# Optimization experiments

Hardware: AMD Instinct MI355X
Metric: run time of the kernel (lower is better)

## Reference

```python
import jax, jax.numpy as jnp
import numpy as np
import math

# config constants (match init_kwargs)
H = 1024; NH = 16; NKV = 4; HD = 64; E = 16; I = 512
NG = 4; TKG = 2; TK = 4; ROUTED_SCALE = 2.5; EPS = 1e-6; THETA = 10000.0
B = 2; S = 1024


def setup_inputs() -> dict:
    key = jax.random.key(0)
    ks = jax.random.split(key, 16)
    sd = 0.02
    inp = {
        "hidden_states": jax.random.normal(ks[0], (B, S, H), jnp.float32),
        "position_ids": jnp.arange(B * S, dtype=jnp.int64).reshape(B, S) % 4096,
        "ln1_w": jnp.ones((H,), jnp.float32),
        "ln2_w": jnp.ones((H,), jnp.float32),
        "q_w": jax.random.normal(ks[1], (NH * HD, H), jnp.float32) * sd,
        "k_w": jax.random.normal(ks[2], (NKV * HD, H), jnp.float32) * sd,
        "v_w": jax.random.normal(ks[3], (NKV * HD, H), jnp.float32) * sd,
        "o_w": jax.random.normal(ks[4], (H, NH * HD), jnp.float32) * sd,
        "gate_w": jax.random.normal(ks[5], (E, H), jnp.float32) * sd,
        "e_bias": jax.random.normal(ks[6], (E,), jnp.float32) * 0.1,
        "W_gu": jax.random.normal(ks[7], (E, 2 * I, H), jnp.float32) * sd,
        "W_d": jax.random.normal(ks[8], (E, H, I), jnp.float32) * sd,
        "sg_w": jax.random.normal(ks[9], (2 * I, H), jnp.float32) * sd,
        "su_w": jax.random.normal(ks[10], (2 * I, H), jnp.float32) * sd,
        "sd_w": jax.random.normal(ks[11], (H, 2 * I), jnp.float32) * sd,
    }
    return inp


def _rmsnorm(x, w, eps=EPS):
    v = jnp.mean(x.astype(jnp.float32) ** 2, axis=-1, keepdims=True)
    return w * (x * jax.lax.rsqrt(v + eps)).astype(w.dtype)


def _rotate_half(x):
    x1, x2 = x[..., : HD // 2], x[..., HD // 2 :]
    return jnp.concatenate([-x2, x1], axis=-1)


def _attention(hs, position_ids, q_w, k_w, v_w, o_w):
    b, s, _ = hs.shape
    q = (hs @ q_w.T).reshape(b, s, NH, HD).transpose(0, 2, 1, 3)   # [B,NH,S,HD]
    k = (hs @ k_w.T).reshape(b, s, NKV, HD).transpose(0, 2, 1, 3)
    v = (hs @ v_w.T).reshape(b, s, NKV, HD).transpose(0, 2, 1, 3)
    # RoPE
    inv_freq = 1.0 / (THETA ** (jnp.arange(0, HD, 2, dtype=jnp.float32) / HD))
    freqs = position_ids.astype(jnp.float32)[..., None] * inv_freq  # [B,S,HD/2]
    emb = jnp.concatenate([freqs, freqs], axis=-1)                  # [B,S,HD]
    cos = jnp.cos(emb)[:, None]                                     # [B,1,S,HD]
    sin = jnp.sin(emb)[:, None]
    q = q * cos + _rotate_half(q) * sin
    k = k * cos + _rotate_half(k) * sin
    # GQA: repeat kv heads
    groups = NH // NKV
    k = jnp.repeat(k, groups, axis=1)
    v = jnp.repeat(v, groups, axis=1)
    scale = 1.0 / math.sqrt(HD)
    scores = jnp.einsum("bhsd,bhtd->bhst", q, k) * scale
    causal = jnp.triu(jnp.full((s, s), -jnp.inf, jnp.float32), k=1)
    scores = scores + causal[None, None]
    attn = jax.nn.softmax(scores.astype(jnp.float32), axis=-1).astype(q.dtype)
    out = jnp.einsum("bhst,bhtd->bhsd", attn, v)
    out = out.transpose(0, 2, 1, 3).reshape(b, s, NH * HD)
    return out @ o_w.T


def _moe(x, gate_w, e_bias, W_gu, W_d, sg_w, su_w, sd_w):
    b, s, h = x.shape
    xf = x.reshape(-1, h)                                     # [T,H]
    T = xf.shape[0]
    logits = xf.astype(jnp.float32) @ gate_w.astype(jnp.float32).T  # [T,E]
    scores = jax.nn.sigmoid(logits)
    sfc = scores + e_bias[None]
    # group-restricted top-k
    gsize = E // NG
    group_scores = sfc.reshape(T, NG, gsize).max(axis=-1)     # [T,NG]
    _, gidx = jax.lax.top_k(group_scores, TKG)                # [T,TKG]
    gmask = jnp.zeros((T, NG), bool).at[jnp.arange(T)[:, None], gidx].set(True)
    smask = jnp.repeat(gmask, gsize, axis=1)                  # [T,E]
    masked = jnp.where(smask, sfc, 0.0)
    _, topk_idx = jax.lax.top_k(masked, TK)                   # [T,TK]
    topk_w = jnp.take_along_axis(scores, topk_idx, axis=1)    # [T,TK]
    topk_w = topk_w / (topk_w.sum(axis=-1, keepdims=True) + 1e-20)
    topk_w = (topk_w * ROUTED_SCALE).astype(xf.dtype)
    # combine weights [T,E] (scatter-add over selected experts)
    combine = jnp.zeros((T, E), xf.dtype).at[
        jnp.arange(T)[:, None], topk_idx].add(topk_w)
    # dense expert compute (static shapes), weighted combine fused in einsum
    gu = jnp.einsum("th,eih->tei", xf, W_gu)                  # [T,E,2I]
    hidden = jax.nn.silu(gu[..., :I]) * gu[..., I:]           # [T,E,I]
    routed = jnp.einsum("tei,ehi,te->th", hidden, W_d, combine)
    # shared experts
    shared = ((jax.nn.silu(xf @ sg_w.T) * (xf @ su_w.T)) @ sd_w.T)
    return (routed + shared).reshape(b, s, h)


def reference(hidden_states, position_ids, ln1_w, ln2_w, q_w, k_w, v_w, o_w,
              gate_w, e_bias, W_gu, W_d, sg_w, su_w, sd_w):
    res = hidden_states
    hs = _rmsnorm(hidden_states, ln1_w)
    hs = res + _attention(hs, position_ids, q_w, k_w, v_w, o_w)
    res = hs
    hs = _rmsnorm(hs, ln2_w)
    hs = res + _moe(hs, gate_w, e_bias, W_gu, W_d, sg_w, su_w, sd_w)
    return hs
```

## Files before the change

kernel.cpp:

```cpp
#include <hip/hip_runtime.h>
#include <hip/hip_bf16.h>
#include <stdint.h>

typedef float f32x4 __attribute__((ext_vector_type(4)));
typedef short s16x8 __attribute__((ext_vector_type(8)));
typedef short s16x4 __attribute__((ext_vector_type(4)));

__device__ __forceinline__ short f2bf(float x) {
    union { float f; uint32_t u; } v; v.f = x;
    uint32_t r = v.u + 0x7fffu + ((v.u >> 16) & 1u);
    return (short)(r >> 16);
}
__device__ __forceinline__ float bf2f(short b) {
    union { uint32_t u; float f; } v; v.u = ((uint32_t)(uint16_t)b) << 16;
    return v.f;
}
__device__ __forceinline__ void gld16(const void* g, void* l) {
    __builtin_amdgcn_global_load_lds((const __attribute__((address_space(1))) uint32_t*)g,
                                     (__attribute__((address_space(3))) uint32_t*)l, 16, 0, 0);
}

__global__ __launch_bounds__(256) void cvt_small_kernel(const float* __restrict__ q, const float* __restrict__ k,
                                                        const float* __restrict__ v, const float* __restrict__ sg,
                                                        const float* __restrict__ su, short* __restrict__ wqkv,
                                                        short* __restrict__ wsgsu) {
    size_t i = (size_t)blockIdx.x * 256 + threadIdx.x;
    const float* src; short* dst;
    if (i < 131072) { src = q + i * 8; dst = wqkv + i * 8; }
    else if (i < 163840) { src = k + (i - 131072) * 8; dst = wqkv + 1048576 + (i - 131072) * 8; }
    else if (i < 196608) { src = v + (i - 163840) * 8; dst = wqkv + 1310720 + (i - 163840) * 8; }
    else if (i < 327680) { src = sg + (i - 196608) * 8; dst = wsgsu + (i - 196608) * 8; }
    else { src = su + (i - 327680) * 8; dst = wsgsu + 1048576 + (i - 327680) * 8; }
    f32x4 a = ((const f32x4*)src)[0];
    f32x4 b = ((const f32x4*)src)[1];
    s16x8 o8;
    o8[0] = f2bf(a[0]); o8[1] = f2bf(a[1]); o8[2] = f2bf(a[2]); o8[3] = f2bf(a[3]);
    o8[4] = f2bf(b[0]); o8[5] = f2bf(b[1]); o8[6] = f2bf(b[2]); o8[7] = f2bf(b[3]);
    *(s16x8*)dst = o8;
}

__global__ __launch_bounds__(256) void rmsnorm_kernel(const float* __restrict__ x, const float* __restrict__ w,
                                                      short* __restrict__ out) {
    int t = blockIdx.x;
    f32x4 v = ((const f32x4*)(x + (size_t)t * 1024))[threadIdx.x];
    float ssq = v[0]*v[0] + v[1]*v[1] + v[2]*v[2] + v[3]*v[3];
#pragma unroll
    for (int o = 1; o < 64; o <<= 1) ssq += __shfl_xor(ssq, o);
    __shared__ float red[4];
    if ((threadIdx.x & 63) == 0) red[threadIdx.x >> 6] = ssq;
    __syncthreads();
    float tot = red[0] + red[1] + red[2] + red[3];
    float rs = rsqrtf(tot * (1.0f / 1024.0f) + 1e-6f);
    f32x4 wv = ((const f32x4*)w)[threadIdx.x];
    s16x4 o4;
#pragma unroll
    for (int j = 0; j < 4; ++j) o4[j] = f2bf(v[j] * rs * wv[j]);
    ((s16x4*)(out + (size_t)t * 1024))[threadIdx.x] = o4;
}

__global__ __launch_bounds__(256) void addnorm_kernel(const float* __restrict__ a, const short* __restrict__ b,
                                                      const float* __restrict__ w, float* __restrict__ res,
                                                      short* __restrict__ xf, float* __restrict__ xf32) {
    int t = blockIdx.x;
    f32x4 va = ((const f32x4*)(a + (size_t)t * 1024))[threadIdx.x];
    f32x4 vb = {0.f, 0.f, 0.f, 0.f};
#pragma unroll
    for (int z = 0; z < 4; ++z) {
        s16x4 dz = *(const s16x4*)(b + (size_t)z * 2048 * 1024 + (size_t)t * 1024 + threadIdx.x * 4);
#pragma unroll
        for (int j = 0; j < 4; ++j) vb[j] += bf2f(dz[j]);
    }
    f32x4 s = va + vb;
    ((f32x4*)(res + (size_t)t * 1024))[threadIdx.x] = s;
    float ssq = s[0]*s[0] + s[1]*s[1] + s[2]*s[2] + s[3]*s[3];
#pragma unroll
    for (int o = 1; o < 64; o <<= 1) ssq += __shfl_xor(ssq, o);
    __shared__ float red[4];
    if ((threadIdx.x & 63) == 0) red[threadIdx.x >> 6] = ssq;
    __syncthreads();
    float tot = red[0] + red[1] + red[2] + red[3];
    float rs = rsqrtf(tot * (1.0f / 1024.0f) + 1e-6f);
    f32x4 wv = ((const f32x4*)w)[threadIdx.x];
    f32x4 xo;
    s16x4 o4;
#pragma unroll
    for (int j = 0; j < 4; ++j) { xo[j] = s[j] * rs * wv[j]; o4[j] = f2bf(xo[j]); }
    ((f32x4*)(xf32 + (size_t)t * 1024))[threadIdx.x] = xo;
    ((s16x4*)(xf + (size_t)t * 1024))[threadIdx.x] = o4;
}

__global__ __launch_bounds__(256, 4) void gemm2_kernel(const short* __restrict__ A, const short* __restrict__ Bg,
                                                       void* __restrict__ Cv, int M, int N, int Ktot, int Ksub,
                                                       long long cstride,
                                                       const int* __restrict__ counts, const int* __restrict__ lists,
                                                       const int* __restrict__ plan, int a_shift, int store_bf16) {
    __shared__ short As[2][128 * 32];
    __shared__ short Bs[2][128 * 32];
    int e, bm, bn, k0, Mloc;
    size_t coff = (size_t)blockIdx.z * cstride;
    const int* rl = nullptr;
    if (plan) {
        int wi = blockIdx.y;
        if (wi >= plan[0]) return;
        int it = plan[1 + wi];
        e = it & 31; bm = (it >> 5) * 128;
        bn = blockIdx.x * 128;
        Mloc = counts[e]; rl = lists + e * 2048;
    } else {
        e = 0; bm = blockIdx.x * 128; bn = blockIdx.y * 128;
        Mloc = M;
    }
    k0 = blockIdx.z * Ksub;
    if (bm >= Mloc) return;
    const short* Bt = Bg + (size_t)e * N * Ktot;
    int tid = threadIdx.x, w = tid >> 6, l = tid & 63;
    int lr = l & 15, lg = l >> 4;
    int rsub = l >> 2, u = l & 3;
    int fs = (rsub & 3) ^ ((rsub >> 2) & 3);
    int colsel = (u ^ fs) * 8;
    int ra = w * 32 + rsub;
    int ga0 = bm + ra;       if (ga0 > Mloc - 1) ga0 = Mloc - 1;
    int ga1 = bm + ra + 16;  if (ga1 > Mloc - 1) ga1 = Mloc - 1;
    int ar0 = rl ? (rl[ga0] >> a_shift) : ga0;
    int ar1 = rl ? (rl[ga1] >> a_shift) : ga1;
    const short* Ap0 = A + (size_t)ar0 * Ktot + k0 + colsel;
    const short* Ap1 = A + (size_t)ar1 * Ktot + k0 + colsel;
    const short* Bp0 = Bt + (size_t)(bn + ra) * Ktot + k0 + colsel;
    const short* Bp1 = Bt + (size_t)(bn + ra + 16) * Ktot + k0 + colsel;
    int lb0 = w * 1024, lb1 = w * 1024 + 512;

    int wm = (w >> 1) * 64, wn = (w & 1) * 64;
    int su = lg ^ (lr & 3) ^ ((lr >> 2) & 3);
    int aoff[4], boff[4];
#pragma unroll
    for (int mf = 0; mf < 4; ++mf) aoff[mf] = (wm + mf * 16 + lr) * 32 + su * 8;
#pragma unroll
    for (int nf = 0; nf < 4; ++nf) boff[nf] = (wn + nf * 16 + lr) * 32 + su * 8;

    f32x4 zero4 = {0.f, 0.f, 0.f, 0.f};
    f32x4 acc[4][4];
#pragma unroll
    for (int mf = 0; mf < 4; ++mf)
#pragma unroll
        for (int nf = 0; nf < 4; ++nf) acc[mf][nf] = zero4;

#define STAGE(buf, kt) do { \
        gld16(Ap0 + (kt) * 32, &As[buf][lb0]); \
        gld16(Ap1 + (kt) * 32, &As[buf][lb1]); \
        gld16(Bp0 + (kt) * 32, &Bs[buf][lb0]); \
        gld16(Bp1 + (kt) * 32, &Bs[buf][lb1]); \
    } while (0)

    int nk = Ksub >> 5;
    STAGE(0, 0);
    asm volatile("s_waitcnt vmcnt(0)");
    __syncthreads();
    for (int kt = 0; kt < nk; ++kt) {
        int cur = kt & 1;
        if (kt + 1 < nk) STAGE(cur ^ 1, kt + 1);
        s16x8 af[4], bfr[4];
#pragma unroll
        for (int mf = 0; mf < 4; ++mf) af[mf] = *(const s16x8*)&As[cur][aoff[mf]];
#pragma unroll
        for (int nf = 0; nf < 4; ++nf) bfr[nf] = *(const s16x8*)&Bs[cur][boff[nf]];
#pragma unroll
        for (int mf = 0; mf < 4; ++mf)
#pragma unroll
            for (int nf = 0; nf < 4; ++nf)
                acc[mf][nf] = __builtin_amdgcn_mfma_f32_16x16x32_bf16(af[mf], bfr[nf], acc[mf][nf], 0, 0, 0);
        __syncthreads();
    }
#undef STAGE
    float* Cf = (float*)Cv;
    short* Cs = (short*)Cv;
#pragma unroll
    for (int mf = 0; mf < 4; ++mf) {
        int rbase = bm + wm + mf * 16 + lg * 4;
#pragma unroll
        for (int r = 0; r < 4; ++r) {
            int grow = rbase + r;
            if (grow < Mloc) {
                int crow = rl ? rl[grow] : grow;
                size_t cb = coff + (size_t)crow * N + bn + wn + lr;
                if (store_bf16) {
#pragma unroll
                    for (int nf = 0; nf < 4; ++nf) Cs[cb + nf * 16] = f2bf(acc[mf][nf][r]);
                } else {
#pragma unroll
                    for (int nf = 0; nf < 4; ++nf) Cf[cb + nf * 16] = acc[mf][nf][r];
                }
            }
        }
    }
}

__global__ __launch_bounds__(256, 3) void gemm3_kernel(const short* __restrict__ A, const float* __restrict__ Bg,
                                                       void* __restrict__ Cv, int M, int N, int Ktot, int Ksub,
                                                       long long cstride,
                                                       const int* __restrict__ counts, const int* __restrict__ lists,
                                                       const int* __restrict__ plan, int a_shift, int store_bf16) {
    __shared__ short As[2][128 * 32];
    __shared__ short Bs[2][128 * 32];
    int e, bm, bn, k0, Mloc;
    size_t coff = (size_t)blockIdx.z * cstride;
    const int* rl = nullptr;
    if (plan) {
        int wi = blockIdx.y;
        if (wi >= plan[0]) return;
        int it = plan[1 + wi];
        e = it & 31; bm = (it >> 5) * 128;
        bn = blockIdx.x * 128;
        Mloc = counts[e]; rl = lists + e * 2048;
    } else {
        e = 0; bm = blockIdx.x * 128; bn = blockIdx.y * 128;
        Mloc = M;
    }
    k0 = blockIdx.z * Ksub;
    if (bm >= Mloc) return;
    const float* Bt = Bg + (size_t)e * N * Ktot;
    int tid = threadIdx.x, w = tid >> 6, l = tid & 63;
    int lr = l & 15, lg = l >> 4;
    int rsub = l >> 2, u = l & 3;
    int fs = (rsub & 3) ^ ((rsub >> 2) & 3);
    int colsel = (u ^ fs) * 8;
    int ra = w * 32 + rsub;
    int ga0 = bm + ra;       if (ga0 > Mloc - 1) ga0 = Mloc - 1;
    int ga1 = bm + ra + 16;  if (ga1 > Mloc - 1) ga1 = Mloc - 1;
    int ar0 = rl ? (rl[ga0] >> a_shift) : ga0;
    int ar1 = rl ? (rl[ga1] >> a_shift) : ga1;
    const short* Ap0 = A + (size_t)ar0 * Ktot + k0 + colsel;
    const short* Ap1 = A + (size_t)ar1 * Ktot + k0 + colsel;
    const float* Bp0 = Bt + (size_t)(bn + ra) * Ktot + k0 + u * 8;
    const float* Bp1 = Bt + (size_t)(bn + ra + 16) * Ktot + k0 + u * 8;
    int lb0 = w * 1024, lb1 = w * 1024 + 512;
    int sb0 = w * 1024 + rsub * 32 + colsel, sb1 = sb0 + 512;

    int wm = (w >> 1) * 64, wn = (w & 1) * 64;
    int su = lg ^ (lr & 3) ^ ((lr >> 2) & 3);
    int aoff[4], boff[4];
#pragma unroll
    for (int mf = 0; mf < 4; ++mf) aoff[mf] = (wm + mf * 16 + lr) * 32 + su * 8;
#pragma unroll
    for (int nf = 0; nf < 4; ++nf) boff[nf] = (wn + nf * 16 + lr) * 32 + su * 8;

    f32x4 zero4 = {0.f, 0.f, 0.f, 0.f};
    f32x4 acc[4][4];
#pragma unroll
    for (int mf = 0; mf < 4; ++mf)
#pragma unroll
        for (int nf = 0; nf < 4; ++nf) acc[mf][nf] = zero4;

    f32x4 b00, b01, b10, b11;
#define BLOAD(kt) do { \
        const float* p0 = Bp0 + (kt) * 32; const float* p1 = Bp1 + (kt) * 32; \
        b00 = *(const f32x4*)p0; b01 = *(const f32x4*)(p0 + 4); \
        b10 = *(const f32x4*)p1; b11 = *(const f32x4*)(p1 + 4); \
    } while (0)
#define BWRITE(buf) do { \
        s16x8 t0, t1; \
        t0[0] = f2bf(b00[0]); t0[1] = f2bf(b00[1]); t0[2] = f2bf(b00[2]); t0[3] = f2bf(b00[3]); \
        t0[4] = f2bf(b01[0]); t0[5] = f2bf(b01[1]); t0[6] = f2bf(b01[2]); t0[7] = f2bf(b01[3]); \
        t1[0] = f2bf(b10[0]); t1[1] = f2bf(b10[1]); t1[2] = f2bf(b10[2]); t1[3] = f2bf(b10[3]); \
        t1[4] = f2bf(b11[0]); t1[5] = f2bf(b11[1]); t1[6] = f2bf(b11[2]); t1[7] = f2bf(b11[3]); \
        *(s16x8*)&Bs[buf][sb0] = t0; *(s16x8*)&Bs[buf][sb1] = t1; \
    } while (0)
#define ASTAGE(buf, kt) do { \
        gld16(Ap0 + (kt) * 32, &As[buf][lb0]); \
        gld16(Ap1 + (kt) * 32, &As[buf][lb1]); \
    } while (0)

    int nk = Ksub >> 5;
    BLOAD(0); ASTAGE(0, 0); BWRITE(0);
    asm volatile("s_waitcnt vmcnt(0)");
    __syncthreads();
    for (int kt = 0; kt < nk; ++kt) {
        int cur = kt & 1;
        if (kt + 1 < nk) { BLOAD(kt + 1); ASTAGE(cur ^ 1, kt + 1); }
        s16x8 af[4], bfr[4];
#pragma unroll
        for (int mf = 0; mf < 4; ++mf) af[mf] = *(const s16x8*)&As[cur][aoff[mf]];
#pragma unroll
        for (int nf = 0; nf < 4; ++nf) bfr[nf] = *(const s16x8*)&Bs[cur][boff[nf]];
#pragma unroll
        for (int mf = 0; mf < 4; ++mf)
#pragma unroll
            for (int nf = 0; nf < 4; ++nf)
                acc[mf][nf] = __builtin_amdgcn_mfma_f32_16x16x32_bf16(af[mf], bfr[nf], acc[mf][nf], 0, 0, 0);
        if (kt + 1 < nk) BWRITE(cur ^ 1);
        __syncthreads();
    }
#undef BLOAD
#undef BWRITE
#undef ASTAGE
    float* Cf = (float*)Cv;
    short* Cs = (short*)Cv;
#pragma unroll
    for (int mf = 0; mf < 4; ++mf) {
        int rbase = bm + wm + mf * 16 + lg * 4;
#pragma unroll
        for (int r = 0; r < 4; ++r) {
            int grow = rbase + r;
            if (grow < Mloc) {
                int crow = rl ? rl[grow] : grow;
                size_t cb = coff + (size_t)crow * N + bn + wn + lr;
                if (store_bf16) {
#pragma unroll
                    for (int nf = 0; nf < 4; ++nf) Cs[cb + nf * 16] = f2bf(acc[mf][nf][r]);
                } else {
#pragma unroll
                    for (int nf = 0; nf < 4; ++nf) Cf[cb + nf * 16] = acc[mf][nf][r];
                }
            }
        }
    }
}

__global__ __launch_bounds__(64) void rope_kernel(const short* __restrict__ qkv, short* __restrict__ Qr,
                                                  short* __restrict__ Kr, short* __restrict__ Vt) {
    int t = blockIdx.x;
    int b = t >> 10, s = t & 1023;
    int l = threadIdx.x;
    __shared__ float cs[32], sn[32], row[1536];
    float acc[24];
#pragma unroll
    for (int c = 0; c < 24; ++c) acc[c] = 0.f;
#pragma unroll
    for (int z = 0; z < 4; ++z) {
        const short* src = qkv + (size_t)z * 2048 * 1536 + (size_t)t * 1536 + l * 24;
#pragma unroll
        for (int c8 = 0; c8 < 3; ++c8) {
            s16x8 v8 = *(const s16x8*)(src + c8 * 8);
#pragma unroll
            for (int j = 0; j < 8; ++j) acc[c8 * 8 + j] += bf2f(v8[j]);
        }
    }
#pragma unroll
    for (int c = 0; c < 24; ++c) row[l * 24 + c] = acc[c];
    if (l < 32) {
        float fr = (float)t * exp2f(-(float)l * 0.41524101186f);
        cs[l] = cosf(fr); sn[l] = sinf(fr);
    }
    __syncthreads();
    int d = l;
    float c = cs[d & 31], sv = sn[d & 31];
#pragma unroll
    for (int h = 0; h < 16; ++h) {
        float x = row[h * 64 + d];
        float rot = (d < 32) ? -row[h * 64 + d + 32] : row[h * 64 + d - 32];
        Qr[((size_t)(b * 16 + h) * 1024 + s) * 64 + d] = f2bf((x * c + rot * sv) * 0.125f);
    }
#pragma unroll
    for (int h = 0; h < 4; ++h) {
        float x = row[1024 + h * 64 + d];
        float rot = (d < 32) ? -row[1024 + h * 64 + d + 32] : row[1024 + h * 64 + d - 32];
        Kr[((size_t)(b * 4 + h) * 1024 + s) * 64 + d] = f2bf(x * c + rot * sv);
        Vt[((size_t)(b * 4 + h) * 64 + d) * 1024 + s] = f2bf(row[1280 + h * 64 + d]);
    }
}

struct KV { s16x8 k[4]; s16x8 v[4]; };
__device__ __forceinline__ void kv_load(KV& r, const short* Kb, const short* Vb, int k0, int lr, int lg) {
    const short* K0 = Kb + (size_t)(k0 + lr) * 64 + lg * 8;
    const short* K1 = Kb + (size_t)(k0 + 16 + lr) * 64 + lg * 8;
    r.k[0] = *(const s16x8*)K0;
    r.k[1] = *(const s16x8*)(K0 + 32);
    r.k[2] = *(const s16x8*)K1;
    r.k[3] = *(const s16x8*)(K1 + 32);
#pragma unroll
    for (int dt = 0; dt < 4; ++dt)
        r.v[dt] = *(const s16x8*)(Vb + (size_t)(dt * 16 + lr) * 1024 + k0 + lg * 8);
}
__device__ __forceinline__ void chain_step(const KV& kv, s16x8 qf0, s16x8 qf1, f32x4* o,
                                           float& m, float& lsum, short* Pl,
                                           int lr, int lg, int k0, int qmask) {
    f32x4 z = {0.f, 0.f, 0.f, 0.f};
    f32x4 sc0 = z, sc1 = z;
    sc0 = __builtin_amdgcn_mfma_f32_16x16x32_bf16(kv.k[0], qf0, sc0, 0, 0, 0);
    sc0 = __builtin_amdgcn_mfma_f32_16x16x32_bf16(kv.k[1], qf1, sc0, 0, 0, 0);
    sc1 = __builtin_amdgcn_mfma_f32_16x16x32_bf16(kv.k[2], qf0, sc1, 0, 0, 0);
    sc1 = __builtin_amdgcn_mfma_f32_16x16x32_bf16(kv.k[3], qf1, sc1, 0, 0, 0);
#pragma unroll
    for (int r = 0; r < 4; ++r) {
        if (k0 + lg * 4 + r > qmask) sc0[r] = -1e30f;
        if (k0 + 16 + lg * 4 + r > qmask) sc1[r] = -1e30f;
    }
    float tm = fmaxf(fmaxf(fmaxf(sc0[0], sc0[1]), fmaxf(sc0[2], sc0[3])),
                     fmaxf(fmaxf(sc1[0], sc1[1]), fmaxf(sc1[2], sc1[3])));
    tm = fmaxf(tm, __shfl_xor(tm, 16));
    tm = fmaxf(tm, __shfl_xor(tm, 32));
    float newm = fmaxf(m, tm);
    float fac = __expf(m - newm);
    float p[8];
#pragma unroll
    for (int r = 0; r < 4; ++r) { p[r] = __expf(sc0[r] - newm); p[4 + r] = __expf(sc1[r] - newm); }
    float ts = ((p[0] + p[1]) + (p[2] + p[3])) + ((p[4] + p[5]) + (p[6] + p[7]));
    ts += __shfl_xor(ts, 16);
    ts += __shfl_xor(ts, 32);
    lsum = lsum * fac + ts;
    m = newm;
    s16x4 w0, w1;
#pragma unroll
    for (int r = 0; r < 4; ++r) { w0[r] = f2bf(p[r]); w1[r] = f2bf(p[4 + r]); }
    *(s16x4*)&Pl[lr * 40 + lg * 4] = w0;
    *(s16x4*)&Pl[lr * 40 + 16 + lg * 4] = w1;
    s16x8 pf = *(const s16x8*)&Pl[lr * 40 + lg * 8];
#pragma unroll
    for (int dt = 0; dt < 4; ++dt) {
        o[dt] *= fac;
        o[dt] = __builtin_amdgcn_mfma_f32_16x16x32_bf16(kv.v[dt], pf, o[dt], 0, 0, 0);
    }
}

__global__ __launch_bounds__(64) void attn_kernel(const short* __restrict__ Qr, const short* __restrict__ Kr,
                                                  const short* __restrict__ Vt, short* __restrict__ attn_out) {
    int p = blockIdx.x;
    int hb = blockIdx.y;
    int b = hb >> 4, h = hb & 15, kv = h >> 2;
    int l = threadIdx.x;
    int lr = l & 15, lg = l >> 4;
    int q0A = p * 16, q0B = (63 - p) * 16;
    __shared__ short PlA[16 * 40], PlB[16 * 40];
    const short* Qh = Qr + (size_t)(b * 16 + h) * 1024 * 64;
    s16x8 qA0 = *(const s16x8*)(Qh + (size_t)(q0A + lr) * 64 + lg * 8);
    s16x8 qA1 = *(const s16x8*)(Qh + (size_t)(q0A + lr) * 64 + 32 + lg * 8);
    s16x8 qB0 = *(const s16x8*)(Qh + (size_t)(q0B + lr) * 64 + lg * 8);
    s16x8 qB1 = *(const s16x8*)(Qh + (size_t)(q0B + lr) * 64 + 32 + lg * 8);
    const short* Kbase = Kr + (size_t)(b * 4 + kv) * 1024 * 64;
    const short* Vbase = Vt + (size_t)(b * 4 + kv) * 64 * 1024;

    f32x4 zero4 = {0.f, 0.f, 0.f, 0.f};
    f32x4 oA[4], oB[4];
#pragma unroll
    for (int dt = 0; dt < 4; ++dt) { oA[dt] = zero4; oB[dt] = zero4; }
    float mA = -1e30f, lsA = 0.f, mB = -1e30f, lsB = 0.f;
    int ntA = (q0A + 47) >> 5, ntB = (q0B + 47) >> 5;
    int qmA = q0A + lr, qmB = q0B + lr;
    const int BIG = 1 << 29;

    KV b0, b1;
    kv_load(b0, Kbase, Vbase, 0, lr, lg);
    for (int kt = 0; kt < ntB; kt += 2) {
        if (kt + 1 < ntB) kv_load(b1, Kbase, Vbase, (kt + 1) * 32, lr, lg);
        if (kt < ntA) chain_step(b0, qA0, qA1, oA, mA, lsA, PlA, lr, lg, kt * 32,
                                 (kt == ntA - 1) ? qmA : BIG);
        chain_step(b0, qB0, qB1, oB, mB, lsB, PlB, lr, lg, kt * 32,
                   (kt == ntB - 1) ? qmB : BIG);
        if (kt + 1 >= ntB) break;
        if (kt + 2 < ntB) kv_load(b0, Kbase, Vbase, (kt + 2) * 32, lr, lg);
        if (kt + 1 < ntA) chain_step(b1, qA0, qA1, oA, mA, lsA, PlA, lr, lg, (kt + 1) * 32,
                                     (kt + 1 == ntA - 1) ? qmA : BIG);
        chain_step(b1, qB0, qB1, oB, mB, lsB, PlB, lr, lg, (kt + 1) * 32,
                   (kt + 1 == ntB - 1) ? qmB : BIG);
    }
    float invA = 1.f / lsA, invB = 1.f / lsB;
    short* oa = attn_out + ((size_t)(b * 1024 + q0A + lr)) * 1024 + h * 64;
    short* ob = attn_out + ((size_t)(b * 1024 + q0B + lr)) * 1024 + h * 64;
#pragma unroll
    for (int dt = 0; dt < 4; ++dt)
#pragma unroll
        for (int r = 0; r < 4; ++r) {
            oa[dt * 16 + lg * 4 + r] = f2bf(oA[dt][r] * invA);
            ob[dt * 16 + lg * 4 + r] = f2bf(oB[dt][r] * invB);
        }
}

__global__ __launch_bounds__(256) void router_topk_kernel(const float* __restrict__ x32, const float* __restrict__ gw,
                                                          const float* __restrict__ eb, float* __restrict__ tw,
                                                          int* __restrict__ tidx) {
    int t = blockIdx.x * 4 + (threadIdx.x >> 6);
    int l = threadIdx.x & 63;
    const float* x = x32 + (size_t)t * 1024;
    f32x4 xv[4];
#pragma unroll
    for (int j = 0; j < 4; ++j) xv[j] = *(const f32x4*)(x + j * 256 + l * 4);
    float acc[16];
#pragma unroll
    for (int e = 0; e < 16; ++e) {
        float a = 0.f;
#pragma unroll
        for (int j = 0; j < 4; ++j) {
            f32x4 g = *(const f32x4*)(gw + (size_t)e * 1024 + j * 256 + l * 4);
            a += xv[j][0]*g[0] + xv[j][1]*g[1] + xv[j][2]*g[2] + xv[j][3]*g[3];
        }
        acc[e] = a;
    }
#pragma unroll
    for (int e = 0; e < 16; ++e) {
#pragma unroll
        for (int o = 1; o < 64; o <<= 1) acc[e] += __shfl_xor(acc[e], o);
    }
    if (l == 0) {
        float score[16], sfc[16];
#pragma unroll
        for (int e = 0; e < 16; ++e) {
            score[e] = 1.f / (1.f + __expf(-acc[e]));
            sfc[e] = score[e] + eb[e];
        }
        float gs[4];
#pragma unroll
        for (int g = 0; g < 4; ++g)
            gs[g] = fmaxf(fmaxf(sfc[4 * g], sfc[4 * g + 1]), fmaxf(sfc[4 * g + 2], sfc[4 * g + 3]));
        int g1 = 0;
        for (int g = 1; g < 4; ++g) if (gs[g] > gs[g1]) g1 = g;
        int g2 = -1;
        for (int g = 0; g < 4; ++g) {
            if (g == g1) continue;
            if (g2 < 0 || gs[g] > gs[g2]) g2 = g;
        }
        float masked[16];
#pragma unroll
        for (int e = 0; e < 16; ++e) {
            int g = e >> 2;
            masked[e] = (g == g1 || g == g2) ? sfc[e] : 0.0f;
        }
        float tot = 1e-20f;
        int idx[4]; float wv[4];
        for (int k = 0; k < 4; ++k) {
            int bi = 0;
            float bv = -1e30f;
            for (int e2 = 0; e2 < 16; ++e2)
                if (masked[e2] > bv) { bv = masked[e2]; bi = e2; }
            idx[k] = bi;
            wv[k] = score[bi];
            masked[bi] = -1e30f;
            tot += wv[k];
        }
        for (int k = 0; k < 4; ++k) {
            tw[t * 4 + k] = wv[k] / tot * 2.5f;
            tidx[t * 4 + k] = idx[k];
        }
    }
}

__global__ __launch_bounds__(64) void router_lists_kernel(const int* __restrict__ tidx, int* __restrict__ counts,
                                                          int* __restrict__ lists) {
    int e = blockIdx.x;
    int l = threadIdx.x;
    int base = 0;
    for (int it = 0; it < 128; ++it) {
        int p = it * 64 + l;
        bool match = (tidx[p] == e);
        unsigned long long mask = __ballot(match);
        int pos = __popcll(mask & ((1ull << l) - 1ull));
        if (match) lists[e * 2048 + base + pos] = p;
        base += __popcll(mask);
    }
    if (l == 0) counts[e] = base;
}

__global__ void plan_kernel(const int* __restrict__ counts, int* __restrict__ plan) {
    if (threadIdx.x == 0) {
        int n = 0;
        for (int e = 0; e < 16; ++e) {
            int nb = (counts[e] + 127) >> 7;
            for (int m2 = 0; m2 < nb; ++m2) plan[1 + n++] = e | (m2 << 5);
        }
        plan[0] = n;
    }
}

__global__ __launch_bounds__(128) void silu_routed_kernel(const short* __restrict__ gu, short* __restrict__ hid) {
    int pr = blockIdx.x;
    int j = threadIdx.x * 4;
    float g[4] = {0.f, 0.f, 0.f, 0.f}, u2[4] = {0.f, 0.f, 0.f, 0.f};
#pragma unroll
    for (int z = 0; z < 2; ++z) {
        const short* base = gu + (size_t)z * 8192 * 1024 + (size_t)pr * 1024;
        s16x4 gz = *(const s16x4*)(base + j);
        s16x4 uz = *(const s16x4*)(base + 512 + j);
#pragma unroll
        for (int k = 0; k < 4; ++k) { g[k] += bf2f(gz[k]); u2[k] += bf2f(uz[k]); }
    }
    s16x4 o;
#pragma unroll
    for (int k = 0; k < 4; ++k) o[k] = f2bf(g[k] / (1.f + __expf(-g[k])) * u2[k]);
    *(s16x4*)(hid + (size_t)pr * 512 + j) = o;
}

__global__ __launch_bounds__(256) void silu_shared_kernel(const short* __restrict__ gu, short* __restrict__ h) {
    int t = blockIdx.x;
    int j = threadIdx.x * 4;
    float g[4] = {0.f, 0.f, 0.f, 0.f}, u2[4] = {0.f, 0.f, 0.f, 0.f};
#pragma unroll
    for (int z = 0; z < 2; ++z) {
        const short* base = gu + (size_t)z * 2048 * 2048 + (size_t)t * 2048;
        s16x4 gz = *(const s16x4*)(base + j);
        s16x4 uz = *(const s16x4*)(base + 1024 + j);
#pragma unroll
        for (int k = 0; k < 4; ++k) { g[k] += bf2f(gz[k]); u2[k] += bf2f(uz[k]); }
    }
    s16x4 o;
#pragma unroll
    for (int k = 0; k < 4; ++k) o[k] = f2bf(g[k] / (1.f + __expf(-g[k])) * u2[k]);
    *(s16x4*)(h + (size_t)t * 1024 + j) = o;
}

__global__ __launch_bounds__(256) void combine_kernel(const float* __restrict__ res2, const short* __restrict__ sdp,
                                                      const short* __restrict__ slots, const float* __restrict__ tw,
                                                      float* __restrict__ out) {
    int t = blockIdx.x;
    int i = threadIdx.x;
    f32x4 acc = ((const f32x4*)(res2 + (size_t)t * 1024))[i];
#pragma unroll
    for (int z = 0; z < 4; ++z) {
        s16x4 d = *(const s16x4*)(sdp + (size_t)z * 2048 * 1024 + (size_t)t * 1024 + i * 4);
#pragma unroll
        for (int j = 0; j < 4; ++j) acc[j] += bf2f(d[j]);
    }
#pragma unroll
    for (int s = 0; s < 4; ++s) {
        float w = tw[t * 4 + s];
        s16x4 d = ((const s16x4*)(slots + (size_t)(t * 4 + s) * 1024))[i];
#pragma unroll
        for (int j = 0; j < 4; ++j) acc[j] += bf2f(d[j]) * w;
    }
    ((f32x4*)(out + (size_t)t * 1024))[i] = acc;
}

extern "C" void kernel_launch(void* const* d_in, const int* in_sizes, int n_in,
                              void* d_out, int out_size, void* d_ws, size_t ws_size,
                              hipStream_t stream) {
    const float* hidden = (const float*)d_in[0];
    const float* ln1 = (const float*)d_in[2];
    const float* ln2 = (const float*)d_in[3];
    const float* qw = (const float*)d_in[4];
    const float* kw = (const float*)d_in[5];
    const float* vw = (const float*)d_in[6];
    const float* ow = (const float*)d_in[7];
    const float* gatew = (const float*)d_in[8];
    const float* ebias = (const float*)d_in[9];
    const float* wgu = (const float*)d_in[10];
    const float* wd = (const float*)d_in[11];
    const float* sgw = (const float*)d_in[12];
    const float* suw = (const float*)d_in[13];
    const float* sdw = (const float*)d_in[14];
    float* out = (float*)d_out;

    char* base = (char*)d_ws;
    size_t off = 0;
    auto alloc = [&](size_t bytes) -> char* {
        char* r = base + off;
        off += (bytes + 255) & ~(size_t)255;
        return r;
    };
    const size_t MB = 1u << 20;

    short* wqkv_b = (short*)alloc((size_t)1536 * 1024 * 2);
    short* wsgsu_b= (short*)alloc((size_t)2048 * 1024 * 2);
    float* res2 = (float*)alloc((size_t)2048 * 1024 * 4);
    short* xf   = (short*)alloc((size_t)2048 * 1024 * 2);
    float* topkw = (float*)alloc(2048 * 4 * 4);
    int* tidx   = (int*)alloc(8192 * 4);
    int* counts = (int*)alloc(64);
    int* lists  = (int*)alloc(16 * 2048 * 4);
    int* plan   = (int*)alloc(512);
    short* shhid = (short*)alloc((size_t)2048 * 1024 * 2);
    short* hid   = (short*)alloc((size_t)8192 * 512 * 2);

    char* ov = alloc(50 * MB);
    short* xn1       = (short*)(ov);
    short* qkv_part  = (short*)(ov + 4 * MB);
    short* Qr        = (short*)(ov);
    short* Kr        = (short*)(ov + 28 * MB);
    short* Vt        = (short*)(ov + 29 * MB);
    short* attn_out  = (short*)(ov + 30 * MB);
    short* attnproj_part = (short*)(ov + 34 * MB);
    float* xf32      = (float*)(ov);
    short* upbuf     = (short*)(ov);
    short* down_slot = (short*)(ov);
    short* sd_part   = (short*)(ov + 16 * MB);

    cvt_small_kernel<<<1792, 256, 0, stream>>>(qw, kw, vw, sgw, suw, wqkv_b, wsgsu_b);

    rmsnorm_kernel<<<2048, 256, 0, stream>>>(hidden, ln1, xn1);
    gemm2_kernel<<<dim3(16, 12, 4), 256, 0, stream>>>(xn1, wqkv_b, qkv_part, 2048, 1536, 1024, 256,
                                                      2048LL * 1536, nullptr, nullptr, nullptr, 0, 1);
    rope_kernel<<<2048, 64, 0, stream>>>(qkv_part, Qr, Kr, Vt);
    attn_kernel<<<dim3(32, 32, 1), 64, 0, stream>>>(Qr, Kr, Vt, attn_out);
    gemm3_kernel<<<dim3(16, 8, 4), 256, 0, stream>>>(attn_out, ow, attnproj_part, 2048, 1024, 1024, 256,
                                                     2048LL * 1024, nullptr, nullptr, nullptr, 0, 1);
    addnorm_kernel<<<2048, 256, 0, stream>>>(hidden, attnproj_part, ln2, res2, xf, xf32);

    router_topk_kernel<<<512, 256, 0, stream>>>(xf32, gatew, ebias, topkw, tidx);
    router_lists_kernel<<<16, 64, 0, stream>>>(tidx, counts, lists);
    plan_kernel<<<1, 64, 0, stream>>>(counts, plan);

    gemm2_kernel<<<dim3(16, 16, 2), 256, 0, stream>>>(xf, wsgsu_b, upbuf, 2048, 2048, 1024, 512,
                                                      2048LL * 2048, nullptr, nullptr, nullptr, 0, 1);
    silu_shared_kernel<<<2048, 256, 0, stream>>>(upbuf, shhid);

    gemm3_kernel<<<dim3(8, 80, 2), 256, 0, stream>>>(xf, wgu, upbuf, 0, 1024, 1024, 512,
                                                     8192LL * 1024, counts, lists, plan, 2, 1);
    silu_routed_kernel<<<8192, 128, 0, stream>>>(upbuf, hid);

    gemm3_kernel<<<dim3(8, 80, 1), 256, 0, stream>>>(hid, wd, down_slot, 0, 1024, 512, 512,
                                                     0LL, counts, lists, plan, 0, 1);
    gemm3_kernel<<<dim3(16, 8, 4), 256, 0, stream>>>(shhid, sdw, sd_part, 2048, 1024, 1024, 256,
                                                     2048LL * 1024, nullptr, nullptr, nullptr, 0, 1);

    combine_kernel<<<2048, 256, 0, stream>>>(res2, sd_part, down_slot, topkw, out);

    (void)in_sizes; (void)n_in; (void)out_size; (void)ws_size;
}
```

Measured before the change: 278.3 us.

## Deepen gemm3 B-register prefetch to two stages with partial vmcnt waits

```diff
diff --git a/kernel.cpp b/kernel.cpp
--- a/kernel.cpp
+++ b/kernel.cpp
@@ -194,7 +194,14 @@
     }
 }
 
-__global__ __launch_bounds__(256, 3) void gemm3_kernel(const short* __restrict__ A, const float* __restrict__ Bg,
+#define WAITBAR4 do { __builtin_amdgcn_sched_barrier(0); \
+        asm volatile("s_waitcnt vmcnt(4) lgkmcnt(0)" ::: "memory"); \
+        __builtin_amdgcn_s_barrier(); __builtin_amdgcn_sched_barrier(0); } while (0)
+#define WAITBAR0 do { __builtin_amdgcn_sched_barrier(0); \
+        asm volatile("s_waitcnt vmcnt(0) lgkmcnt(0)" ::: "memory"); \
+        __builtin_amdgcn_s_barrier(); __builtin_amdgcn_sched_barrier(0); } while (0)
+
+__global__ __launch_bounds__(256, 4) void gemm3_kernel(const short* __restrict__ A, const float* __restrict__ Bg,
                                                        void* __restrict__ Cv, int M, int N, int Ktot, int Ksub,
                                                        long long cstride,
                                                        const int* __restrict__ counts, const int* __restrict__ lists,
@@ -250,48 +257,60 @@
 #pragma unroll
         for (int nf = 0; nf < 4; ++nf) acc[mf][nf] = zero4;
 
-    f32x4 b00, b01, b10, b11;
-#define BLOAD(kt) do { \
+    f32x4 bA00, bA01, bA10, bA11, bB00, bB01, bB10, bB11;
+#define BLOAD(S, kt) do { \
         const float* p0 = Bp0 + (kt) * 32; const float* p1 = Bp1 + (kt) * 32; \
-        b00 = *(const f32x4*)p0; b01 = *(const f32x4*)(p0 + 4); \
-        b10 = *(const f32x4*)p1; b11 = *(const f32x4*)(p1 + 4); \
+        S##00 = *(const f32x4*)p0; S##01 = *(const f32x4*)(p0 + 4); \
+        S##10 = *(const f32x4*)p1; S##11 = *(const f32x4*)(p1 + 4); \
     } while (0)
-#define BWRITE(buf) do { \
+#define BWRITE(S, buf) do { \
         s16x8 t0, t1; \
-        t0[0] = f2bf(b00[0]); t0[1] = f2bf(b00[1]); t0[2] = f2bf(b00[2]); t0[3] = f2bf(b00[3]); \
-        t0[4] = f2bf(b01[0]); t0[5] = f2bf(b01[1]); t0[6] = f2bf(b01[2]); t0[7] = f2bf(b01[3]); \
-        t1[0] = f2bf(b10[0]); t1[1] = f2bf(b10[1]); t1[2] = f2bf(b10[2]); t1[3] = f2bf(b10[3]); \
-        t1[4] = f2bf(b11[0]); t1[5] = f2bf(b11[1]); t1[6] = f2bf(b11[2]); t1[7] = f2bf(b11[3]); \
+        t0[0] = f2bf(S##00[0]); t0[1] = f2bf(S##00[1]); t0[2] = f2bf(S##00[2]); t0[3] = f2bf(S##00[3]); \
+        t0[4] = f2bf(S##01[0]); t0[5] = f2bf(S##01[1]); t0[6] = f2bf(S##01[2]); t0[7] = f2bf(S##01[3]); \
+        t1[0] = f2bf(S##10[0]); t1[1] = f2bf(S##10[1]); t1[2] = f2bf(S##10[2]); t1[3] = f2bf(S##10[3]); \
+        t1[4] = f2bf(S##11[0]); t1[5] = f2bf(S##11[1]); t1[6] = f2bf(S##11[2]); t1[7] = f2bf(S##11[3]); \
         *(s16x8*)&Bs[buf][sb0] = t0; *(s16x8*)&Bs[buf][sb1] = t1; \
     } while (0)
 #define ASTAGE(buf, kt) do { \
         gld16(Ap0 + (kt) * 32, &As[buf][lb0]); \
         gld16(Ap1 + (kt) * 32, &As[buf][lb1]); \
     } while (0)
+#define COMPUTE(buf) do { \
+        s16x8 af[4], bfr[4]; \
+        for (int mf = 0; mf < 4; ++mf) af[mf] = *(const s16x8*)&As[buf][aoff[mf]]; \
+        for (int nf = 0; nf < 4; ++nf) bfr[nf] = *(const s16x8*)&Bs[buf][boff[nf]]; \
+        for (int mf = 0; mf < 4; ++mf) \
+            for (int nf = 0; nf < 4; ++nf) \
+                acc[mf][nf] = __builtin_amdgcn_mfma_f32_16x16x32_bf16(af[mf], bfr[nf], acc[mf][nf], 0, 0, 0); \
+    } while (0)
 
     int nk = Ksub >> 5;
-    BLOAD(0); ASTAGE(0, 0); BWRITE(0);
-    asm volatile("s_waitcnt vmcnt(0)");
-    __syncthreads();
-    for (int kt = 0; kt < nk; ++kt) {
-        int cur = kt & 1;
-        if (kt + 1 < nk) { BLOAD(kt + 1); ASTAGE(cur ^ 1, kt + 1); }
-        s16x8 af[4], bfr[4];
-#pragma unroll
-        for (int mf = 0; mf < 4; ++mf) af[mf] = *(const s16x8*)&As[cur][aoff[mf]];
-#pragma unroll
-        for (int nf = 0; nf < 4; ++nf) bfr[nf] = *(const s16x8*)&Bs[cur][boff[nf]];
-#pragma unroll
-        for (int mf = 0; mf < 4; ++mf)
-#pragma unroll
-            for (int nf = 0; nf < 4; ++nf)
-                acc[mf][nf] = __builtin_amdgcn_mfma_f32_16x16x32_bf16(af[mf], bfr[nf], acc[mf][nf], 0, 0, 0);
-        if (kt + 1 < nk) BWRITE(cur ^ 1);
-        __syncthreads();
+    BLOAD(bA, 0);
+    ASTAGE(0, 0);
+    BWRITE(bA, 0);
+    BLOAD(bB, 1);
+    WAITBAR4;
+    for (int kt = 0; kt < nk; kt += 2) {
+        {
+            if (kt + 1 < nk) ASTAGE(1, kt + 1);
+            if (kt + 2 < nk) BLOAD(bA, kt + 2);
+            COMPUTE(0);
+            if (kt + 1 < nk) BWRITE(bB, 1);
+            if (kt + 2 < nk) { WAITBAR4; } else { WAITBAR0; }
+        }
+        if (kt + 1 >= nk) break;
+        {
+            if (kt + 2 < nk) ASTAGE(0, kt + 2);
+            if (kt + 3 < nk) BLOAD(bB, kt + 3);
+            COMPUTE(1);
+            if (kt + 2 < nk) BWRITE(bA, 0);
+            if (kt + 3 < nk) { WAITBAR4; } else { WAITBAR0; }
+        }
     }
 #undef BLOAD
 #undef BWRITE
 #undef ASTAGE
+#undef COMPUTE
     float* Cf = (float*)Cv;
     short* Cs = (short*)Cv;
 #pragma unroll
```

Result: no change. 278.0 us (-0.1%).
